# Kernel tuning notes

Measured on AMD Instinct MI355X. Metric: run time of the kernel, lower is better.

Reference implementation:

```python
import jax, jax.numpy as jnp
import numpy as np
import math

B, S, H = 4, 2048, 1024
EMBED_DIM = 1024


def setup_inputs() -> dict:
    key = jax.random.key(0)
    ks = jax.random.split(key, 7)
    scale = 1.0 / math.sqrt(H)
    return {
        "xs": jax.random.normal(ks[0], (B, S, H), dtype=jnp.float32),
        "WQ_w": jax.random.normal(ks[1], (EMBED_DIM, H), dtype=jnp.float32) * scale,
        "WQ_b": jax.random.normal(ks[2], (EMBED_DIM,), dtype=jnp.float32) * scale,
        "WK_w": jax.random.normal(ks[3], (EMBED_DIM, H), dtype=jnp.float32) * scale,
        "WK_b": jax.random.normal(ks[4], (EMBED_DIM,), dtype=jnp.float32) * scale,
        "WV_w": jax.random.normal(ks[5], (EMBED_DIM, H), dtype=jnp.float32) * scale,
        "WV_b": jax.random.normal(ks[6], (EMBED_DIM,), dtype=jnp.float32) * scale,
    }


def reference(xs, WQ_w, WQ_b, WK_w, WK_b, WV_w, WV_b):
    # Linear projections (torch nn.Linear: x @ W.T + b)
    q = jnp.einsum('bsh,eh->bse', xs, WQ_w) + WQ_b  # [B,S,E]
    k = jnp.einsum('bsh,eh->bse', xs, WK_w) + WK_b
    v = jnp.einsum('bsh,eh->bse', xs, WV_w) + WV_b
    seq_len = xs.shape[1]
    inv_sqrt_e = 1.0 / math.sqrt(EMBED_DIM)
    qk = jnp.einsum('bqe,bke->bqk', q, k) * inv_sqrt_e  # [B,S,S]
    # causal mask: positions k > q get -inf (triu, diagonal=1)
    causal = jnp.tril(jnp.ones((seq_len, seq_len), dtype=bool))
    qk = jnp.where(causal[None, :, :], qk, -jnp.inf)
    attn = jax.nn.softmax(qk, axis=2)
    y = jnp.einsum('bqk,bke->bqe', attn, v)  # [B,S,E]
    return y
```

## Files before the change

kernel.cpp:

```cpp
#include <hip/hip_runtime.h>
#include <cstdint>
#include <cstddef>

typedef _Float16 f16;
typedef __attribute__((ext_vector_type(4))) _Float16 f16x4;
typedef __attribute__((ext_vector_type(8))) _Float16 f16x8;
typedef __attribute__((ext_vector_type(4))) float f32x4;

static constexpr int BB = 4;
static constexpr int SS = 2048;
static constexpr int EE = 1024;

static constexpr int BM = 128, BN = 128;

__device__ __forceinline__ void gload_lds16(const f16* g, f16* l) {
  __builtin_amdgcn_global_load_lds(
      (const __attribute__((address_space(1))) void*)g,
      (__attribute__((address_space(3))) void*)l, 16, 0, 0);
}

struct Frag {
  int lane, wave, wy, wx, l16, quad, quadx;
  __device__ Frag() {
    const int tid = threadIdx.x;
    lane = tid & 63; wave = tid >> 6;
    wy = wave >> 1; wx = wave & 1;
    l16 = lane & 15; quad = lane >> 4;
    quadx = quad ^ ((l16 >> 2) & 3);
  }
};

struct Stager {
  const f16* g[2];
  int l[2];
  __device__ void init(const f16* base, int ld, const Frag& fr) {
#pragma unroll
    for (int i = 0; i < 2; ++i) {
      const int c = fr.wave * 128 + i * 64 + fr.lane;
      const int row = c >> 2;
      const int kcs = (c & 3) ^ ((c >> 4) & 3);
      g[i] = base + (size_t)row * ld + kcs * 8;
      l[i] = c * 8;
    }
  }
  __device__ __forceinline__ void stage(int ko, f16* lds) const {
    gload_lds16(g[0] + ko, lds + l[0]);
    gload_lds16(g[1] + ko, lds + l[1]);
  }
};

__device__ __forceinline__ void mfma_round(
    const f16* __restrict__ Ash, const f16* __restrict__ Bsh,
    f32x4 acc[4][4], const Frag& fr)
{
  f16x8 af[4], bf[4];
#pragma unroll
  for (int mi = 0; mi < 4; ++mi)
    af[mi] = *(const f16x8*)(Ash + (fr.wy * 64 + mi * 16 + fr.l16) * 32 + fr.quadx * 8);
#pragma unroll
  for (int ni = 0; ni < 4; ++ni)
    bf[ni] = *(const f16x8*)(Bsh + (fr.wx * 64 + ni * 16 + fr.l16) * 32 + fr.quadx * 8);
#pragma unroll
  for (int mi = 0; mi < 4; ++mi)
#pragma unroll
    for (int ni = 0; ni < 4; ++ni)
      acc[mi][ni] = __builtin_amdgcn_mfma_f32_16x16x32_f16(af[mi], bf[ni], acc[mi][ni], 0, 0, 0);
}

__device__ __forceinline__ void gemm_core(
    const f16* __restrict__ A, const f16* __restrict__ Bt,
    int lda, int ldb, int kOuter,
    f16* __restrict__ Ash, f16* __restrict__ Bsh,
    f32x4 acc[4][4], const Frag& fr)
{
  Stager sa, sb;
  sa.init(A, lda, fr);
  sb.init(Bt, ldb, fr);
  for (int kt = 0; kt < kOuter; ++kt) {
    const int ko = kt * 64;
    sa.stage(ko, Ash);       sa.stage(ko + 32, Ash + 128 * 32);
    sb.stage(ko, Bsh);       sb.stage(ko + 32, Bsh + 128 * 32);
    __syncthreads();
    mfma_round(Ash, Bsh, acc, fr);
    mfma_round(Ash + 128 * 32, Bsh + 128 * 32, acc, fr);
    __syncthreads();
  }
}

__global__ __launch_bounds__(256) void cast_all_kernel(
    const float* __restrict__ xs,
    const float* __restrict__ w0, const float* __restrict__ w1, const float* __restrict__ w2,
    f16* __restrict__ Xh, f16* __restrict__ o0, f16* __restrict__ o1, f16* __restrict__ o2)
{
  const int i = blockIdx.x * 256 + threadIdx.x;
  const float* src; f16* dst; int idx;
  if (i < 2097152) {
    src = xs; dst = Xh; idx = i;
  } else {
    const int j = i - 2097152;
    const int w = j >> 18;
    idx = j & 262143;
    src = (w == 0) ? w0 : (w == 1) ? w1 : w2;
    dst = (w == 0) ? o0 : (w == 1) ? o1 : o2;
  }
  const float4 f = ((const float4*)src)[idx];
  f16x4 h;
  h.x = (f16)f.x; h.y = (f16)f.y; h.z = (f16)f.z; h.w = (f16)f.w;
  ((f16x4*)dst)[idx] = h;
}

__global__ __launch_bounds__(512, 1) void proj3_kernel(
    const f16* __restrict__ X,
    const f16* __restrict__ Wq, const f16* __restrict__ Wk, const f16* __restrict__ Wv,
    const float* __restrict__ bq, const float* __restrict__ bk, const float* __restrict__ bv,
    f16* __restrict__ Qh, f16* __restrict__ Kh, f16* __restrict__ Vt)
{
  __shared__ __align__(16) f16 smem[73728];
  const int tid = threadIdx.x;
  const int lane = tid & 63, wave = tid >> 6;
  const int wy = wave >> 1, wx = wave & 1;
  const int l16 = lane & 15, quad = lane >> 4;

  const int t = blockIdx.x;
  const int which = t >> 8;
  const int u = t & 255;
  const int c8 = u & 7, g = u >> 3;
  const f16* Abase; const f16* Bbase;
  int mt, nt;
  if (which < 2) {
    mt = c8 + 8 * (g >> 3);
    nt = g & 7;
    Abase = X + (size_t)mt * 256 * EE;
    Bbase = ((which == 0) ? Wq : Wk) + (size_t)nt * 128 * EE;
  } else {
    mt = g & 3;
    nt = c8 + 8 * (g >> 2);
    Abase = Wv + (size_t)mt * 256 * EE;
    Bbase = X + (size_t)nt * 128 * EE;
  }

  const f16* gA[4]; int lA[4];
  const f16* gB[2]; int lB[2];
#pragma unroll
  for (int j = 0; j < 4; ++j) {
    const int slot = j * 512 + tid;
    const int r = slot >> 3, cg = (slot & 7) ^ (r & 7);
    gA[j] = Abase + (size_t)r * EE + cg * 8;
    lA[j] = slot * 8;
  }
#pragma unroll
  for (int j = 0; j < 2; ++j) {
    const int slot = j * 512 + tid;
    const int r = slot >> 3, cg = (slot & 7) ^ (r & 7);
    gB[j] = Bbase + (size_t)r * EE + cg * 8;
    lB[j] = slot * 8;
  }

  auto stageTile = [&](int bi, int kt) {
    const int ko = kt * 64;
    f16* ab = smem + bi * 16384;
    f16* bb = smem + 49152 + bi * 8192;
    gload_lds16(gA[0] + ko, ab + lA[0]);
    gload_lds16(gA[1] + ko, ab + lA[1]);
    gload_lds16(gA[2] + ko, ab + lA[2]);
    gload_lds16(gA[3] + ko, ab + lA[3]);
    gload_lds16(gB[0] + ko, bb + lB[0]);
    gload_lds16(gB[1] + ko, bb + lB[1]);
  };

  int offA[4][2], offB[4][2];
#pragma unroll
  for (int i = 0; i < 4; ++i)
#pragma unroll
    for (int ks = 0; ks < 2; ++ks) {
      { const int row = wy * 64 + i * 16 + l16, c = ks * 4 + quad;
        offA[i][ks] = (row * 8 + (c ^ (row & 7))) * 8; }
      { const int row = wx * 64 + i * 16 + l16, c = ks * 4 + quad;
        offB[i][ks] = (row * 8 + (c ^ (row & 7))) * 8; }
    }

  stageTile(0, 0);
  stageTile(1, 1);

  f32x4 acc[4][4] = {};

  constexpr int NT = 16;
  int bi = 0;
  for (int kt = 0; kt < NT; ++kt) {
    const int bs = (bi >= 1) ? bi - 1 : bi + 2;
    __builtin_amdgcn_s_barrier();
    if (kt <= NT - 3) stageTile(bs, kt + 2);
    if (kt <= NT - 3)      asm volatile("s_waitcnt vmcnt(12)" ::: "memory");
    else if (kt == NT - 2) asm volatile("s_waitcnt vmcnt(6)" ::: "memory");
    else                   asm volatile("s_waitcnt vmcnt(0)" ::: "memory");
    __builtin_amdgcn_s_barrier();

    const f16* Ac = smem + bi * 16384;
    const f16* Bc = smem + 49152 + bi * 8192;
    f16x8 a[4][2], b[4][2];
#pragma unroll
    for (int mi = 0; mi < 4; ++mi) a[mi][0] = *(const f16x8*)(Ac + offA[mi][0]);
#pragma unroll
    for (int ni = 0; ni < 4; ++ni) b[ni][0] = *(const f16x8*)(Bc + offB[ni][0]);
#pragma unroll
    for (int mi = 0; mi < 4; ++mi) a[mi][1] = *(const f16x8*)(Ac + offA[mi][1]);
#pragma unroll
    for (int ni = 0; ni < 4; ++ni) b[ni][1] = *(const f16x8*)(Bc + offB[ni][1]);

    __builtin_amdgcn_s_setprio(1);
#pragma unroll
    for (int mi = 0; mi < 4; ++mi)
#pragma unroll
      for (int ni = 0; ni < 4; ++ni)
        acc[mi][ni] = __builtin_amdgcn_mfma_f32_16x16x32_f16(a[mi][0], b[ni][0], acc[mi][ni], 0, 0, 0);
#pragma unroll
    for (int mi = 0; mi < 4; ++mi)
#pragma unroll
      for (int ni = 0; ni < 4; ++ni)
        acc[mi][ni] = __builtin_amdgcn_mfma_f32_16x16x32_f16(a[mi][1], b[ni][1], acc[mi][ni], 0, 0, 0);
    __builtin_amdgcn_s_setprio(0);

    bi = (bi == 2) ? 0 : bi + 1;
  }

  const int r0 = mt * 256 + wy * 64;
  const int c0 = nt * 128 + wx * 64;
  if (which < 2) {
    const float* bias = (which == 0) ? bq : bk;
    f16* out = (which == 0) ? Qh : Kh;
#pragma unroll
    for (int ni = 0; ni < 4; ++ni) {
      const int c = c0 + ni * 16 + l16;
      const float bz = bias[c];
#pragma unroll
      for (int mi = 0; mi < 4; ++mi) {
        const int r = r0 + mi * 16 + quad * 4;
#pragma unroll
        for (int i = 0; i < 4; ++i)
          out[(size_t)(r + i) * EE + c] = (f16)(acc[mi][ni][i] + bz);
      }
    }
  } else {
#pragma unroll
    for (int ni = 0; ni < 4; ++ni) {
      const int cg = c0 + ni * 16 + l16;
      const int b = cg >> 11, sc = cg & 2047;
      f16* out = Vt + (size_t)b * EE * SS;
#pragma unroll
      for (int mi = 0; mi < 4; ++mi) {
        const int r = r0 + mi * 16 + quad * 4;
#pragma unroll
        for (int i = 0; i < 4; ++i)
          out[(size_t)(r + i) * SS + sc] = (f16)(acc[mi][ni][i] + bv[r + i]);
      }
    }
  }
}

__global__ __launch_bounds__(256) void scores_kernel(
    const f16* __restrict__ Q, const f16* __restrict__ Kh, f16* __restrict__ Sc)
{
  __shared__ __align__(16) f16 Ash[2][BM * 32];
  __shared__ __align__(16) f16 Bsh[2][BN * 32];
  const int t = blockIdx.x, b = blockIdx.z;
  int qt = 0;
  while ((qt + 1) * (qt + 2) / 2 <= t) ++qt;
  const int kt = t - qt * (qt + 1) / 2;
  const f16* A  = Q  + (size_t)b * SS * EE + (size_t)qt * BM * EE;
  const f16* Bp = Kh + (size_t)b * SS * EE + (size_t)kt * BN * EE;
  f16* out = Sc + (size_t)b * SS * SS;
  Frag fr;
  f32x4 acc[4][4] = {};
  gemm_core(A, Bp, EE, EE, EE / 64, Ash[0], Bsh[0], acc, fr);
  const float scale = 0.03125f;
#pragma unroll
  for (int ni = 0; ni < 4; ++ni) {
    const int c = kt * BN + fr.wx * 64 + ni * 16 + fr.l16;
#pragma unroll
    for (int mi = 0; mi < 4; ++mi) {
      const int r = qt * BM + fr.wy * 64 + mi * 16 + fr.quad * 4;
#pragma unroll
      for (int i = 0; i < 4; ++i)
        out[(size_t)(r + i) * SS + c] = (f16)(acc[mi][ni][i] * scale);
    }
  }
}

__global__ __launch_bounds__(256) void softmax_kernel(f16* __restrict__ Sc)
{
  const int q = blockIdx.x, b = blockIdx.y;
  f16* row = Sc + (size_t)b * SS * SS + (size_t)q * SS;
  const int n = q + 1;
  const int kend = ((q >> 7) + 1) << 7;
  const int tid = threadIdx.x;
  const int i0 = tid * 8;

  float v[8];
  if (i0 + 8 <= n) {
    const f16x8 h = *(const f16x8*)(row + i0);
#pragma unroll
    for (int j = 0; j < 8; ++j) v[j] = (float)h[j];
  } else {
#pragma unroll
    for (int j = 0; j < 8; ++j) {
      const int idx = i0 + j;
      v[j] = (idx < n) ? (float)row[idx] : -1e30f;
    }
  }

  float m = v[0];
#pragma unroll
  for (int j = 1; j < 8; ++j) m = fmaxf(m, v[j]);
  __shared__ float red[4];
#pragma unroll
  for (int off = 32; off > 0; off >>= 1) m = fmaxf(m, __shfl_down(m, off));
  if ((tid & 63) == 0) red[tid >> 6] = m;
  __syncthreads();
  m = fmaxf(fmaxf(red[0], red[1]), fmaxf(red[2], red[3]));

  float sum = 0.f;
#pragma unroll
  for (int j = 0; j < 8; ++j) {
    v[j] = (i0 + j < n) ? __expf(v[j] - m) : 0.f;
    sum += v[j];
  }
#pragma unroll
  for (int off = 32; off > 0; off >>= 1) sum += __shfl_down(sum, off);
  __syncthreads();
  if ((tid & 63) == 0) red[tid >> 6] = sum;
  __syncthreads();
  sum = red[0] + red[1] + red[2] + red[3];
  const float inv = 1.f / sum;

  if (i0 < kend) {
    f16x8 h;
#pragma unroll
    for (int j = 0; j < 8; ++j) h[j] = (f16)(v[j] * inv);
    *(f16x8*)(row + i0) = h;
  }
}

__global__ __launch_bounds__(256) void pv_kernel(
    const f16* __restrict__ P, const f16* __restrict__ Vt, float* __restrict__ Y)
{
  __shared__ __align__(16) f16 Ash[2][BM * 32];
  __shared__ __align__(16) f16 Bsh[2][BN * 32];
  const int t = blockIdx.x;
  const int u = t & 255;
  const int qh = u & 7, et = (u >> 3) & 7, b = u >> 6;
  const int qt = (t < 256) ? (15 - qh) : qh;
  const f16* A  = P  + (size_t)b * SS * SS + (size_t)qt * BM * SS;
  const f16* Bp = Vt + (size_t)b * EE * SS + (size_t)et * BN * SS;
  float* out = Y + (size_t)b * SS * EE;
  Frag fr;
  f32x4 acc[4][4] = {};
  gemm_core(A, Bp, SS, SS, (qt + 1) * 2, Ash[0], Bsh[0], acc, fr);
#pragma unroll
  for (int ni = 0; ni < 4; ++ni) {
    const int c = et * BN + fr.wx * 64 + ni * 16 + fr.l16;
#pragma unroll
    for (int mi = 0; mi < 4; ++mi) {
      const int r = qt * BM + fr.wy * 64 + mi * 16 + fr.quad * 4;
#pragma unroll
      for (int i = 0; i < 4; ++i)
        out[(size_t)(r + i) * EE + c] = acc[mi][ni][i];
    }
  }
}

extern "C" void kernel_launch(void* const* d_in, const int* in_sizes, int n_in,
                              void* d_out, int out_size, void* d_ws, size_t ws_size,
                              hipStream_t stream)
{
  const float* xs  = (const float*)d_in[0];
  const float* WQw = (const float*)d_in[1];
  const float* WQb = (const float*)d_in[2];
  const float* WKw = (const float*)d_in[3];
  const float* WKb = (const float*)d_in[4];
  const float* WVw = (const float*)d_in[5];
  const float* WVb = (const float*)d_in[6];

  const size_t ME = (size_t)BB * SS * EE;
  const size_t WE = (size_t)EE * EE;

  f16* Xh = (f16*)d_ws;
  f16* Wq = Xh + ME;
  f16* Wk = Wq + WE;
  f16* Wv = Wk + WE;
  f16* Qh = Wv + WE;
  f16* Kh = Qh + ME;
  f16* Vt = Kh + ME;
  f16* Sc = Vt + ME;

  cast_all_kernel<<<dim3(11264), 256, 0, stream>>>(
      xs, WQw, WKw, WVw, Xh, Wq, Wk, Wv);

  proj3_kernel<<<dim3(768), 512, 0, stream>>>(
      Xh, Wq, Wk, Wv, WQb, WKb, WVb, Qh, Kh, Vt);

  const int nTri = (SS / BM) * (SS / BM + 1) / 2;
  scores_kernel<<<dim3(nTri, 1, BB), 256, 0, stream>>>(Qh, Kh, Sc);

  softmax_kernel<<<dim3(SS, BB), 256, 0, stream>>>(Sc);

  pv_kernel<<<dim3(512), 256, 0, stream>>>(Sc, Vt, (float*)d_out);
}
```

Baseline: 255.6 us.

## Enlarge projection GEMM tiles to 256x256 with double buffering

The fused QKV projection kernel moves from 256x128 output tiles with triple-buffered LDS to 256x256 tiles with double buffering. The grid drops from 768 to 384 blocks, and the 8 waves are rearranged as 2x4, each computing 128x64. Larger tiles raise operand reuse and cut global loads per MFMA. The trade-off is higher register pressure from the 8x4 accumulators, a shallower prefetch pipeline, and 384 blocks, which may leave some of the 256 CUs idle in a second wave.

After: 261.4 us. +2.3%, slower.

```diff
diff --git a/kernel.cpp b/kernel.cpp
--- a/kernel.cpp
+++ b/kernel.cpp
@@ -109,122 +109,102 @@
   ((f16x4*)dst)[idx] = h;
 }
 
-__global__ __launch_bounds__(512, 1) void proj3_kernel(
+__global__ __launch_bounds__(512, 1) void proj4_kernel(
     const f16* __restrict__ X,
     const f16* __restrict__ Wq, const f16* __restrict__ Wk, const f16* __restrict__ Wv,
     const float* __restrict__ bq, const float* __restrict__ bk, const float* __restrict__ bv,
     f16* __restrict__ Qh, f16* __restrict__ Kh, f16* __restrict__ Vt)
 {
-  __shared__ __align__(16) f16 smem[73728];
+  __shared__ __align__(16) f16 smem[65536];
   const int tid = threadIdx.x;
   const int lane = tid & 63, wave = tid >> 6;
-  const int wy = wave >> 1, wx = wave & 1;
+  const int wy = wave >> 2, wx = wave & 3;
   const int l16 = lane & 15, quad = lane >> 4;
 
   const int t = blockIdx.x;
-  const int which = t >> 8;
-  const int u = t & 255;
+  const int which = (t < 128) ? 0 : (t < 256) ? 1 : 2;
+  const int u = t - which * 128;
   const int c8 = u & 7, g = u >> 3;
   const f16* Abase; const f16* Bbase;
   int mt, nt;
   if (which < 2) {
-    mt = c8 + 8 * (g >> 3);
-    nt = g & 7;
+    mt = c8 + 8 * (g & 3);
+    nt = g >> 2;
     Abase = X + (size_t)mt * 256 * EE;
-    Bbase = ((which == 0) ? Wq : Wk) + (size_t)nt * 128 * EE;
+    Bbase = ((which == 0) ? Wq : Wk) + (size_t)nt * 256 * EE;
   } else {
-    mt = g & 3;
-    nt = c8 + 8 * (g >> 2);
+    nt = c8 + 8 * (g & 3);
+    mt = g >> 2;
     Abase = Wv + (size_t)mt * 256 * EE;
-    Bbase = X + (size_t)nt * 128 * EE;
-  }
-
-  const f16* gA[4]; int lA[4];
-  const f16* gB[2]; int lB[2];
+    Bbase = X + (size_t)nt * 256 * EE;
+  }
+
+  const f16* gA[4]; const f16* gB[4]; int lc[4];
 #pragma unroll
   for (int j = 0; j < 4; ++j) {
     const int slot = j * 512 + tid;
     const int r = slot >> 3, cg = (slot & 7) ^ (r & 7);
     gA[j] = Abase + (size_t)r * EE + cg * 8;
-    lA[j] = slot * 8;
-  }
-#pragma unroll
-  for (int j = 0; j < 2; ++j) {
-    const int slot = j * 512 + tid;
-    const int r = slot >> 3, cg = (slot & 7) ^ (r & 7);
     gB[j] = Bbase + (size_t)r * EE + cg * 8;
-    lB[j] = slot * 8;
+    lc[j] = slot * 8;
   }
 
   auto stageTile = [&](int bi, int kt) {
     const int ko = kt * 64;
     f16* ab = smem + bi * 16384;
-    f16* bb = smem + 49152 + bi * 8192;
-    gload_lds16(gA[0] + ko, ab + lA[0]);
-    gload_lds16(gA[1] + ko, ab + lA[1]);
-    gload_lds16(gA[2] + ko, ab + lA[2]);
-    gload_lds16(gA[3] + ko, ab + lA[3]);
-    gload_lds16(gB[0] + ko, bb + lB[0]);
-    gload_lds16(gB[1] + ko, bb + lB[1]);
+    f16* bb = smem + 32768 + bi * 16384;
+#pragma unroll
+    for (int j = 0; j < 4; ++j) gload_lds16(gA[j] + ko, ab + lc[j]);
+#pragma unroll
+    for (int j = 0; j < 4; ++j) gload_lds16(gB[j] + ko, bb + lc[j]);
   };
 
-  int offA[4][2], offB[4][2];
-#pragma unroll
-  for (int i = 0; i < 4; ++i)
+  int obA[2], obB[2];
+#pragma unroll
+  for (int ks = 0; ks < 2; ++ks) {
+    const int rA = wy * 128 + l16;
+    const int rB = wx * 64 + l16;
+    obA[ks] = (rA * 8 + ((ks * 4 + quad) ^ (rA & 7))) * 8;
+    obB[ks] = (rB * 8 + ((ks * 4 + quad) ^ (rB & 7))) * 8;
+  }
+
+  stageTile(0, 0);
+
+  f32x4 acc[8][4] = {};
+
+  constexpr int NT = 16;
+  for (int kt = 0; kt < NT; ++kt) {
+    const int cur = kt & 1, nxt = cur ^ 1;
+    __builtin_amdgcn_s_barrier();
+    if (kt + 1 < NT) {
+      stageTile(nxt, kt + 1);
+      asm volatile("s_waitcnt vmcnt(8)" ::: "memory");
+    } else {
+      asm volatile("s_waitcnt vmcnt(0)" ::: "memory");
+    }
+    __builtin_amdgcn_s_barrier();
+
+    const f16* Ac = smem + cur * 16384;
+    const f16* Bc = smem + 32768 + cur * 16384;
 #pragma unroll
     for (int ks = 0; ks < 2; ++ks) {
-      { const int row = wy * 64 + i * 16 + l16, c = ks * 4 + quad;
-        offA[i][ks] = (row * 8 + (c ^ (row & 7))) * 8; }
-      { const int row = wx * 64 + i * 16 + l16, c = ks * 4 + quad;
-        offB[i][ks] = (row * 8 + (c ^ (row & 7))) * 8; }
-    }
-
-  stageTile(0, 0);
-  stageTile(1, 1);
-
-  f32x4 acc[4][4] = {};
-
-  constexpr int NT = 16;
-  int bi = 0;
-  for (int kt = 0; kt < NT; ++kt) {
-    const int bs = (bi >= 1) ? bi - 1 : bi + 2;
-    __builtin_amdgcn_s_barrier();
-    if (kt <= NT - 3) stageTile(bs, kt + 2);
-    if (kt <= NT - 3)      asm volatile("s_waitcnt vmcnt(12)" ::: "memory");
-    else if (kt == NT - 2) asm volatile("s_waitcnt vmcnt(6)" ::: "memory");
-    else                   asm volatile("s_waitcnt vmcnt(0)" ::: "memory");
-    __builtin_amdgcn_s_barrier();
-
-    const f16* Ac = smem + bi * 16384;
-    const f16* Bc = smem + 49152 + bi * 8192;
-    f16x8 a[4][2], b[4][2];
-#pragma unroll
-    for (int mi = 0; mi < 4; ++mi) a[mi][0] = *(const f16x8*)(Ac + offA[mi][0]);
-#pragma unroll
-    for (int ni = 0; ni < 4; ++ni) b[ni][0] = *(const f16x8*)(Bc + offB[ni][0]);
-#pragma unroll
-    for (int mi = 0; mi < 4; ++mi) a[mi][1] = *(const f16x8*)(Ac + offA[mi][1]);
-#pragma unroll
-    for (int ni = 0; ni < 4; ++ni) b[ni][1] = *(const f16x8*)(Bc + offB[ni][1]);
-
-    __builtin_amdgcn_s_setprio(1);
-#pragma unroll
-    for (int mi = 0; mi < 4; ++mi)
-#pragma unroll
-      for (int ni = 0; ni < 4; ++ni)
-        acc[mi][ni] = __builtin_amdgcn_mfma_f32_16x16x32_f16(a[mi][0], b[ni][0], acc[mi][ni], 0, 0, 0);
-#pragma unroll
-    for (int mi = 0; mi < 4; ++mi)
-#pragma unroll
-      for (int ni = 0; ni < 4; ++ni)
-        acc[mi][ni] = __builtin_amdgcn_mfma_f32_16x16x32_f16(a[mi][1], b[ni][1], acc[mi][ni], 0, 0, 0);
-    __builtin_amdgcn_s_setprio(0);
-
-    bi = (bi == 2) ? 0 : bi + 1;
-  }
-
-  const int r0 = mt * 256 + wy * 64;
-  const int c0 = nt * 128 + wx * 64;
+      f16x8 a[8], b[4];
+#pragma unroll
+      for (int mi = 0; mi < 8; ++mi) a[mi] = *(const f16x8*)(Ac + obA[ks] + mi * 1024);
+#pragma unroll
+      for (int ni = 0; ni < 4; ++ni) b[ni] = *(const f16x8*)(Bc + obB[ks] + ni * 1024);
+      __builtin_amdgcn_s_setprio(1);
+#pragma unroll
+      for (int mi = 0; mi < 8; ++mi)
+#pragma unroll
+        for (int ni = 0; ni < 4; ++ni)
+          acc[mi][ni] = __builtin_amdgcn_mfma_f32_16x16x32_f16(a[mi], b[ni], acc[mi][ni], 0, 0, 0);
+      __builtin_amdgcn_s_setprio(0);
+    }
+  }
+
+  const int r0 = mt * 256 + wy * 128;
+  const int c0 = nt * 256 + wx * 64;
   if (which < 2) {
     const float* bias = (which == 0) ? bq : bk;
     f16* out = (which == 0) ? Qh : Kh;
@@ -233,7 +213,7 @@
       const int c = c0 + ni * 16 + l16;
       const float bz = bias[c];
 #pragma unroll
-      for (int mi = 0; mi < 4; ++mi) {
+      for (int mi = 0; mi < 8; ++mi) {
         const int r = r0 + mi * 16 + quad * 4;
 #pragma unroll
         for (int i = 0; i < 4; ++i)
@@ -247,7 +227,7 @@
       const int b = cg >> 11, sc = cg & 2047;
       f16* out = Vt + (size_t)b * EE * SS;
 #pragma unroll
-      for (int mi = 0; mi < 4; ++mi) {
+      for (int mi = 0; mi < 8; ++mi) {
         const int r = r0 + mi * 16 + quad * 4;
 #pragma unroll
         for (int i = 0; i < 4; ++i)
@@ -395,7 +375,7 @@
   cast_all_kernel<<<dim3(11264), 256, 0, stream>>>(
       xs, WQw, WKw, WVw, Xh, Wq, Wk, Wv);
 
-  proj3_kernel<<<dim3(768), 512, 0, stream>>>(
+  proj4_kernel<<<dim3(384), 512, 0, stream>>>(
       Xh, Wq, Wk, Wv, WQb, WKb, WVb, Qh, Kh, Vt);
 
   const int nTri = (SS / BM) * (SS / BM + 1) / 2;
```
